# Kernel tuning notes

Measured on AMD Instinct MI355X. Metric: run time of the kernel, lower is better.

The kernel has to match this reference:

```python
import jax, jax.numpy as jnp
import numpy as np

D_MODEL, D_STATE, D_CONV, EXPAND = 1024, 16, 4, 2
D_INNER = EXPAND * D_MODEL
B, L = 2, 4096
LN_EPS = 1e-5


def setup_inputs() -> dict:
    key = jax.random.key(0)
    ks = jax.random.split(key, 6)
    x = jax.random.normal(ks[0], (B, L, D_MODEL), dtype=jnp.float32)
    ln_gamma = jnp.ones((D_MODEL,), jnp.float32)
    ln_beta = jnp.zeros((D_MODEL,), jnp.float32)
    W_in = jax.random.normal(ks[1], (2 * D_INNER, D_MODEL), jnp.float32) / np.sqrt(D_MODEL).astype(np.float32)
    conv_w = jax.random.normal(ks[2], (D_INNER, 1, D_CONV), jnp.float32) * 0.1
    conv_b = jnp.zeros((D_INNER,), jnp.float32)
    W_out = jax.random.normal(ks[3], (D_MODEL, D_INNER), jnp.float32) / np.sqrt(D_INNER).astype(np.float32)
    A = jnp.eye(D_STATE, dtype=jnp.float32)
    Bm = jax.random.normal(ks[4], (D_STATE, D_INNER), jnp.float32) * 0.01
    Cm = jax.random.normal(ks[5], (D_STATE, D_INNER), jnp.float32) * 0.01
    return dict(x=x, ln_gamma=ln_gamma, ln_beta=ln_beta, W_in=W_in,
                conv_w=conv_w, conv_b=conv_b, W_out=W_out, A=A, Bm=Bm, Cm=Cm)


def _layernorm(x, gamma, beta):
    mu = jnp.mean(x, axis=-1, keepdims=True)
    var = jnp.mean(jnp.square(x - mu), axis=-1, keepdims=True)
    return (x - mu) * jax.lax.rsqrt(var + LN_EPS) * gamma + beta


def _causal_depthwise_conv(xp, conv_w, conv_b):
    # xp: (B, L, D_INNER) -> torch Conv1d(padding=K-1, groups=C) then slice [:L]
    # == left-pad K-1, valid depthwise conv.
    lhs = jnp.pad(xp.transpose(0, 2, 1), ((0, 0), (0, 0), (D_CONV - 1, 0)))  # (B,C,L+K-1)
    out = jax.lax.conv_general_dilated(
        lhs, conv_w, window_strides=(1,), padding='VALID',
        dimension_numbers=('NCH', 'OIH', 'NCH'), feature_group_count=D_INNER)
    return out.transpose(0, 2, 1) + conv_b  # (B, L, C)


def reference(x, ln_gamma, ln_beta, W_in, conv_w, conv_b, W_out, A, Bm, Cm):
    # scan permutation is identity (untrained optimizer state); masking disabled
    xn = _layernorm(x, ln_gamma, ln_beta)
    xz = jnp.einsum('bld,ed->ble', xn, W_in)          # (B, L, 2*D_INNER)
    x_part, z = jnp.split(xz, 2, axis=-1)             # each (B, L, D_INNER)
    x_conv = jax.nn.silu(_causal_depthwise_conv(x_part, conv_w, conv_b))

    # recurrence: s_t = s_{t-1} @ A.T + u_t @ B.T ; out_t = (x_conv_t + s_t @ C) * sigmoid(z_t)
    u_seq = x_part.transpose(1, 0, 2)                 # (L, B, D_INNER)
    xc_seq = x_conv.transpose(1, 0, 2)
    z_seq = z.transpose(1, 0, 2)

    def step(state, inp):
        u_t, xc_t, z_t = inp
        state = state @ A.T + u_t @ Bm.T              # (B, D_STATE)
        out = (xc_t + state @ Cm) * jax.nn.sigmoid(z_t)
        return state, out

    state0 = jnp.zeros((x.shape[0], D_STATE), x.dtype)
    _, ys = jax.lax.scan(step, state0, (u_seq, xc_seq, z_seq))
    y = ys.transpose(1, 0, 2)                         # (B, L, D_INNER)
    residual = jnp.einsum('bli,di->bld', y, W_out)    # (B, L, D_MODEL)
    return x + residual
```

## Files before the change

### kernel.cpp

```cpp
#include <hip/hip_runtime.h>
#include <hip/hip_bf16.h>
#include <math.h>

#define D_MODEL 1024
#define D_STATE 16
#define D_CONV 4
#define D_INNER 2048
#define BATCH 2
#define SEQ 4096
#define NROW (BATCH * SEQ)
#define LN_EPS 1e-5f

typedef __attribute__((ext_vector_type(8))) short  bf16x8_t;
typedef __attribute__((ext_vector_type(4))) float  f32x4_t;
typedef __attribute__((ext_vector_type(8))) unsigned short u16x8_t;

__device__ inline unsigned short f2bf(float f) {
    unsigned u = __float_as_uint(f);
    u += 0x7fffu + ((u >> 16) & 1u);
    return (unsigned short)(u >> 16);
}
__device__ inline float bf2f(unsigned short u) {
    return __uint_as_float((unsigned)u << 16);
}

#define GLL16(g, l)                                                            \
    __builtin_amdgcn_global_load_lds(                                          \
        (const __attribute__((address_space(1))) void*)(g),                    \
        (__attribute__((address_space(3))) void*)(l), 16, 0, 0)

#define FENCE asm volatile("" ::: "memory")
#define BAR do { FENCE; __builtin_amdgcn_s_barrier(); FENCE; } while (0)

#define CVT_BLOCKS 3088
__global__ __launch_bounds__(256) void pre_kernel(const float* __restrict__ x,
                                                  const float* __restrict__ gamma,
                                                  const float* __restrict__ beta,
                                                  const float* __restrict__ W_in,
                                                  const float* __restrict__ W_out,
                                                  const float* __restrict__ Bm,
                                                  unsigned short* __restrict__ xn,
                                                  unsigned short* __restrict__ Win_bf,
                                                  unsigned short* __restrict__ Wout_bf,
                                                  unsigned short* __restrict__ Bm_bf) {
    __shared__ float red[8];
    const int tid = threadIdx.x;
    if (blockIdx.x < CVT_BLOCKS) {
        const long long g = (long long)(blockIdx.x * 256 + tid) * 8;
        const long long n1 = (long long)2 * D_INNER * D_MODEL;
        const long long n2 = n1 + (long long)D_MODEL * D_INNER;
        const float* src; unsigned short* dst; long long off;
        if (g < n1)      { src = W_in;  dst = Win_bf;  off = g; }
        else if (g < n2) { src = W_out; dst = Wout_bf; off = g - n1; }
        else             { src = Bm;    dst = Bm_bf;   off = g - n2; }
        const float4 a = *reinterpret_cast<const float4*>(src + off);
        const float4 b = *reinterpret_cast<const float4*>(src + off + 4);
        u16x8_t p;
        p[0] = f2bf(a.x); p[1] = f2bf(a.y); p[2] = f2bf(a.z); p[3] = f2bf(a.w);
        p[4] = f2bf(b.x); p[5] = f2bf(b.y); p[6] = f2bf(b.z); p[7] = f2bf(b.w);
        *reinterpret_cast<u16x8_t*>(dst + off) = p;
        return;
    }
    const int row = blockIdx.x - CVT_BLOCKS;
    const float4* xr = reinterpret_cast<const float4*>(x + (size_t)row * D_MODEL);
    float4 v = xr[tid];

    const int lane = tid & 63, wave = tid >> 6;
    float s = v.x + v.y + v.z + v.w;
    #pragma unroll
    for (int off = 32; off > 0; off >>= 1) s += __shfl_down(s, off, 64);
    if (lane == 0) red[wave] = s;
    __syncthreads();
    float mu = (red[0] + red[1] + red[2] + red[3]) * (1.0f / D_MODEL);
    __syncthreads();

    float dx = v.x - mu, dy = v.y - mu, dz = v.z - mu, dw = v.w - mu;
    float ss = dx * dx + dy * dy + dz * dz + dw * dw;
    #pragma unroll
    for (int off = 32; off > 0; off >>= 1) ss += __shfl_down(ss, off, 64);
    if (lane == 0) red[wave] = ss;
    __syncthreads();
    float var = (red[0] + red[1] + red[2] + red[3]) * (1.0f / D_MODEL);
    float rs = rsqrtf(var + LN_EPS);

    const float4 gv = reinterpret_cast<const float4*>(gamma)[tid];
    const float4 bv = reinterpret_cast<const float4*>(beta)[tid];
    ushort4 o;
    o.x = f2bf(dx * rs * gv.x + bv.x);
    o.y = f2bf(dy * rs * gv.y + bv.y);
    o.z = f2bf(dz * rs * gv.z + bv.z);
    o.w = f2bf(dw * rs * gv.w + bv.w);
    reinterpret_cast<ushort4*>(xn + (size_t)row * D_MODEL)[tid] = o;
}

__global__ __launch_bounds__(512, 2) void gemm256_bf16(const short* __restrict__ A,
                                                       const short* __restrict__ B,
                                                       unsigned short* __restrict__ Cb,
                                                       int M, int N, int K) {
    __shared__ short lds[2 * 4 * 8192];

    const int tid = threadIdx.x;
    const int w = tid >> 6, l = tid & 63;

    const int id = blockIdx.y * gridDim.x + blockIdx.x;
    const int cpx = (gridDim.x * gridDim.y) >> 3;
    const int sid = (id & 7) * cpx + (id >> 3);
    const int row0 = (sid / gridDim.x) * 256;
    const int col0 = (sid % gridDim.x) * 256;

    const int wm = w >> 2;
    const int wn = w & 3;
    const int fr = l & 15;
    const int fc = (l >> 4) * 8;
    const int NT = K >> 6;

    const int qa = wm;
    const int qb = 2 + (wn >> 1);
    const int bb = (wn & 1) * 64;

    auto STAGE = [&](const short* __restrict__ G, int growbase, int k0,
                     int buf, int q) {
        #pragma unroll
        for (int j = 0; j < 2; ++j) {
            const int e = ((j * 8 + w) << 9) + l * 8;
            const int r = e >> 6;
            const int c = (e & 63) ^ ((r & 7) << 3);
            GLL16(G + (size_t)(growbase + r) * K + k0 + c,
                  &lds[buf * 32768 + q * 8192 + ((j * 8 + w) << 9)]);
        }
    };
    auto LDF = [&](int buf, int q, int r, int ks) -> bf16x8_t {
        const int c = (ks * 32 + fc) ^ ((r & 7) << 3);
        return *reinterpret_cast<const bf16x8_t*>(
            &lds[buf * 32768 + q * 8192 + r * 64 + c]);
    };

    f32x4_t acc[8][4] = {};
    bf16x8_t af[4][2], af2[4][2], bA[2][2], bB[2][2];

#define MFMA_Q(AF, mh, nh, BFR)                                                \
    do {                                                                       \
        _Pragma("unroll")                                                      \
        for (int mi = 0; mi < 4; ++mi)                                         \
            _Pragma("unroll")                                                  \
            for (int ni = 0; ni < 2; ++ni)                                     \
                _Pragma("unroll")                                              \
                for (int ks = 0; ks < 2; ++ks)                                 \
                    acc[(mh) * 4 + mi][(nh) * 2 + ni] =                        \
                        __builtin_amdgcn_mfma_f32_16x16x32_bf16(               \
                            AF[mi][ks], BFR[ni][ks],                           \
                            acc[(mh) * 4 + mi][(nh) * 2 + ni], 0, 0, 0);       \
    } while (0)

    STAGE(A, row0,       0, 0, 0);
    STAGE(A, row0 + 128, 0, 0, 1);
    STAGE(B, col0,       0, 0, 2);
    STAGE(B, col0 + 128, 0, 0, 3);
    if (NT > 1) {
        STAGE(B, col0,       64, 1, 2);
        STAGE(B, col0 + 128, 64, 1, 3);
        STAGE(A, row0,       64, 1, 0);
        asm volatile("s_waitcnt vmcnt(6)" ::: "memory");
    } else {
        asm volatile("s_waitcnt vmcnt(0)" ::: "memory");
    }
    BAR;

    for (int kt = 0; kt < NT; ++kt) {
        const int buf = kt & 1, nbuf = buf ^ 1;
        #pragma unroll
        for (int mi = 0; mi < 4; ++mi)
            #pragma unroll
            for (int ks = 0; ks < 2; ++ks)
                af[mi][ks] = LDF(buf, qa, mi * 16 + fr, ks);
        #pragma unroll
        for (int ni = 0; ni < 2; ++ni)
            #pragma unroll
            for (int ks = 0; ks < 2; ++ks)
                bA[ni][ks] = LDF(buf, qb, bb + ni * 16 + fr, ks);
        #pragma unroll
        for (int ni = 0; ni < 2; ++ni)
            #pragma unroll
            for (int ks = 0; ks < 2; ++ks)
                bB[ni][ks] = LDF(buf, qb, bb + 32 + ni * 16 + fr, ks);
        #pragma unroll
        for (int mi = 0; mi < 4; ++mi)
            #pragma unroll
            for (int ks = 0; ks < 2; ++ks)
                af2[mi][ks] = LDF(buf, qa, 64 + mi * 16 + fr, ks);
        if (kt + 1 < NT) STAGE(A, row0 + 128, (kt + 1) << 6, nbuf, 1);
        asm volatile("s_waitcnt lgkmcnt(0)" ::: "memory");
        BAR;
        if (kt + 2 < NT) {
            STAGE(B, col0,       (kt + 2) << 6, buf, 2);
            STAGE(B, col0 + 128, (kt + 2) << 6, buf, 3);
            STAGE(A, row0,       (kt + 2) << 6, buf, 0);
            asm volatile("s_waitcnt vmcnt(6)" ::: "memory");
        } else {
            asm volatile("s_waitcnt vmcnt(0)" ::: "memory");
        }
        BAR;
        __builtin_amdgcn_s_setprio(1);
        MFMA_Q(af,  0, 0, bA);
        MFMA_Q(af,  0, 1, bB);
        MFMA_Q(af2, 1, 1, bB);
        MFMA_Q(af2, 1, 0, bA);
        __builtin_amdgcn_s_setprio(0);
    }
#undef MFMA_Q

    const int cr = (l >> 4) * 4;
    const int cc = l & 15;
    #pragma unroll
    for (int m = 0; m < 8; ++m) {
        #pragma unroll
        for (int n = 0; n < 4; ++n) {
            size_t base = (size_t)(row0 + wm * 128 + m * 16 + cr) * N +
                          (col0 + wn * 64 + n * 16 + cc);
            #pragma unroll
            for (int j = 0; j < 4; ++j)
                Cb[base + (size_t)j * N] = f2bf(acc[m][n][j]);
        }
    }
}

__global__ __launch_bounds__(512) void gemm_out(const short* __restrict__ A,
                                                const short* __restrict__ B,
                                                const float* __restrict__ add,
                                                float* __restrict__ C,
                                                int M, int N, int K) {
    __shared__ short lds[3 * 3 * 8192];

    const int tid = threadIdx.x;
    const int w = tid >> 6, l = tid & 63;

    const int id = blockIdx.y * gridDim.x + blockIdx.x;
    const int cpx = (gridDim.x * gridDim.y) >> 3;
    const int sid = (id & 7) * cpx + (id >> 3);
    const int row0 = (sid / gridDim.x) * 256;
    const int col0 = (sid % gridDim.x) * 128;

    const int wm = w >> 1;
    const int wn = w & 1;
    const int qa = wm >> 1;
    const int lr0 = (wm & 1) * 64;
    const int fr = l & 15;
    const int fc = (l >> 4) * 8;
    const int NT = K >> 6;

    auto STAGE = [&](const short* __restrict__ G, int growbase, int k0,
                     int buf, int q) {
        #pragma unroll
        for (int j = 0; j < 2; ++j) {
            const int e = ((j * 8 + w) << 9) + l * 8;
            const int r = e >> 6;
            const int c = (e & 63) ^ ((r & 7) << 3);
            GLL16(G + (size_t)(growbase + r) * K + k0 + c,
                  &lds[buf * 24576 + q * 8192 + ((j * 8 + w) << 9)]);
        }
    };
    auto LDF = [&](int buf, int q, int r, int ks) -> bf16x8_t {
        const int c = (ks * 32 + fc) ^ ((r & 7) << 3);
        return *reinterpret_cast<const bf16x8_t*>(
            &lds[buf * 24576 + q * 8192 + r * 64 + c]);
    };

    f32x4_t acc[4][4] = {};
    bf16x8_t af[4][2], bf[4][2];

    STAGE(A, row0,       0, 0, 0);
    STAGE(A, row0 + 128, 0, 0, 1);
    STAGE(B, col0,       0, 0, 2);
    if (NT > 1) {
        STAGE(A, row0,       64, 1, 0);
        STAGE(A, row0 + 128, 64, 1, 1);
        STAGE(B, col0,       64, 1, 2);
        asm volatile("s_waitcnt vmcnt(6)" ::: "memory");
    } else {
        asm volatile("s_waitcnt vmcnt(0)" ::: "memory");
    }

    int buf = 0;
    for (int kt = 0; kt < NT; ++kt) {
        BAR;
        #pragma unroll
        for (int mi = 0; mi < 4; ++mi)
            #pragma unroll
            for (int ks = 0; ks < 2; ++ks)
                af[mi][ks] = LDF(buf, qa, lr0 + mi * 16 + fr, ks);
        #pragma unroll
        for (int ni = 0; ni < 4; ++ni)
            #pragma unroll
            for (int ks = 0; ks < 2; ++ks)
                bf[ni][ks] = LDF(buf, 2, wn * 64 + ni * 16 + fr, ks);
        __builtin_amdgcn_s_setprio(1);
        #pragma unroll
        for (int mi = 0; mi < 4; ++mi)
            #pragma unroll
            for (int ni = 0; ni < 4; ++ni)
                #pragma unroll
                for (int ks = 0; ks < 2; ++ks)
                    acc[mi][ni] = __builtin_amdgcn_mfma_f32_16x16x32_bf16(
                        af[mi][ks], bf[ni][ks], acc[mi][ni], 0, 0, 0);
        __builtin_amdgcn_s_setprio(0);
        if (kt + 2 < NT) {
            const int sb = (buf + 2) % 3;
            STAGE(A, row0,       (kt + 2) << 6, sb, 0);
            STAGE(A, row0 + 128, (kt + 2) << 6, sb, 1);
            STAGE(B, col0,       (kt + 2) << 6, sb, 2);
            asm volatile("s_waitcnt vmcnt(6)" ::: "memory");
        } else {
            asm volatile("s_waitcnt vmcnt(0)" ::: "memory");
        }
        buf = (buf + 1) % 3;
    }

    const int cr = (l >> 4) * 4;
    const int cc = l & 15;
    #pragma unroll
    for (int mi = 0; mi < 4; ++mi) {
        #pragma unroll
        for (int ni = 0; ni < 4; ++ni) {
            size_t base = (size_t)(row0 + wm * 64 + mi * 16 + cr) * N +
                          (col0 + wn * 64 + ni * 16 + cc);
            #pragma unroll
            for (int j = 0; j < 4; ++j)
                C[base + (size_t)j * N] = acc[mi][ni][j] + add[base + (size_t)j * N];
        }
    }
}

__global__ __launch_bounds__(64) void v_mfma(const unsigned short* __restrict__ xz,
                                             const unsigned short* __restrict__ Bmb,
                                             float* __restrict__ V) {
    const int l = threadIdx.x;
    const int r0 = blockIdx.x * 16;
    const int fr = l & 15;
    const int fk = (l >> 4) * 8;

    const unsigned short* aP = xz + (size_t)(r0 + fr) * (2 * D_INNER) + fk;
    const unsigned short* bP = Bmb + fr * D_INNER + fk;

    f32x4_t a0 = {}, a1 = {}, a2 = {}, a3 = {};
    #pragma unroll 2
    for (int k0 = 0; k0 < D_INNER; k0 += 128) {
        a0 = __builtin_amdgcn_mfma_f32_16x16x32_bf16(
            *reinterpret_cast<const bf16x8_t*>(aP + k0),
            *reinterpret_cast<const bf16x8_t*>(bP + k0), a0, 0, 0, 0);
        a1 = __builtin_amdgcn_mfma_f32_16x16x32_bf16(
            *reinterpret_cast<const bf16x8_t*>(aP + k0 + 32),
            *reinterpret_cast<const bf16x8_t*>(bP + k0 + 32), a1, 0, 0, 0);
        a2 = __builtin_amdgcn_mfma_f32_16x16x32_bf16(
            *reinterpret_cast<const bf16x8_t*>(aP + k0 + 64),
            *reinterpret_cast<const bf16x8_t*>(bP + k0 + 64), a2, 0, 0, 0);
        a3 = __builtin_amdgcn_mfma_f32_16x16x32_bf16(
            *reinterpret_cast<const bf16x8_t*>(aP + k0 + 96),
            *reinterpret_cast<const bf16x8_t*>(bP + k0 + 96), a3, 0, 0, 0);
    }

    const int cr = (l >> 4) * 4;
    const int cc = l & 15;
    #pragma unroll
    for (int j = 0; j < 4; ++j)
        V[(size_t)(r0 + cr + j) * D_STATE + cc] = a0[j] + a1[j] + a2[j] + a3[j];
}

__global__ __launch_bounds__(256) void scan_par(const float* __restrict__ V,
                                                const float* __restrict__ A,
                                                float* __restrict__ S) {
    __shared__ int nid;
    const int tid = threadIdx.x;
    if (tid == 0) nid = 0;
    __syncthreads();
    {
        const float ex = ((tid >> 4) == (tid & 15)) ? 1.0f : 0.0f;
        if (A[tid] != ex) atomicOr(&nid, 1);
    }
    __syncthreads();
    if (nid) return;

    const int p = blockIdx.x;
    const int b = p >> 4, s = p & 15;
    const float* vb = V + (size_t)b * SEQ * D_STATE + s;
    float* sb = S + (size_t)b * SEQ * D_STATE + s;

    const int t0 = tid * 16;
    float v[16];
    float run = 0.0f;
    #pragma unroll
    for (int j = 0; j < 16; ++j) {
        run += vb[(size_t)(t0 + j) * D_STATE];
        v[j] = run;
    }

    const float tot = run;
    float sc = tot;
    #pragma unroll
    for (int off = 1; off < 64; off <<= 1) {
        float n = __shfl_up(sc, off, 64);
        if ((tid & 63) >= off) sc += n;
    }
    __shared__ float wtot[4];
    if ((tid & 63) == 63) wtot[tid >> 6] = sc;
    __syncthreads();
    float woff = 0.0f;
    #pragma unroll
    for (int w2 = 0; w2 < 4; ++w2)
        if (w2 < (tid >> 6)) woff += wtot[w2];
    const float excl = sc - tot + woff;

    #pragma unroll
    for (int j = 0; j < 16; ++j)
        sb[(size_t)(t0 + j) * D_STATE] = v[j] + excl;
}

#define SCAN_CHUNK 256

__global__ __launch_bounds__(64) void scan_seq(const float* __restrict__ V,
                                               const float* __restrict__ A,
                                               float* __restrict__ S) {
    const int tid = threadIdx.x;
    int bad = 0;
    for (int i = tid; i < D_STATE * D_STATE; i += 64) {
        const float ex = ((i >> 4) == (i & 15)) ? 1.0f : 0.0f;
        if (A[i] != ex) bad = 1;
    }
    if (__ballot(bad) == 0ULL) return;

    __shared__ float Al[D_STATE * D_STATE];
    __shared__ float Vl[2 * SCAN_CHUNK * D_STATE];
    __shared__ float Sl[2 * SCAN_CHUNK * D_STATE];

    for (int i = tid; i < D_STATE * D_STATE; i += 64) Al[i] = A[i];
    __syncthreads();

    float st = 0.0f;
    const int bb = (tid >> 4) & 1;
    const int ss = tid & 15;

    for (int t0 = 0; t0 < SEQ; t0 += SCAN_CHUNK) {
        for (int idx = tid; idx < 2 * SCAN_CHUNK * D_STATE; idx += 64) {
            int b = idx >> 12;
            int rem = idx & 4095;
            Vl[idx] = V[((size_t)(b * SEQ + t0) * D_STATE) + rem];
        }
        __syncthreads();

        if (tid < 32) {
            float* vb = Vl + bb * SCAN_CHUNK * D_STATE + ss;
            float* sb = Sl + bb * SCAN_CHUNK * D_STATE + ss;
            for (int t = 0; t < SCAN_CHUNK; ++t) {
                float ns = vb[t * D_STATE];
                #pragma unroll
                for (int s2 = 0; s2 < D_STATE; ++s2) {
                    float other = __shfl(st, (tid & 16) | s2, 64);
                    ns = fmaf(Al[ss * D_STATE + s2], other, ns);
                }
                st = ns;
                sb[t * D_STATE] = st;
            }
        }
        __syncthreads();

        for (int idx = tid; idx < 2 * SCAN_CHUNK * D_STATE; idx += 64) {
            int b = idx >> 12;
            int rem = idx & 4095;
            S[((size_t)(b * SEQ + t0) * D_STATE) + rem] = Sl[idx];
        }
        __syncthreads();
    }
}

__global__ __launch_bounds__(256) void y_kernel(const unsigned short* __restrict__ xz,
                                                const float* __restrict__ S,
                                                const float* __restrict__ Cm,
                                                const float* __restrict__ convw,
                                                const float* __restrict__ convb,
                                                unsigned short* __restrict__ y) {
    const int tid = threadIdx.x;
    const int i0 = blockIdx.x * 512 + tid * 2;
    const int r0 = blockIdx.y * 64;
    const int tb0 = r0 & (SEQ - 1);

    const float4 w0 = *reinterpret_cast<const float4*>(&convw[i0 * D_CONV]);
    const float4 w1 = *reinterpret_cast<const float4*>(&convw[(i0 + 1) * D_CONV]);
    const float cb0 = convb[i0], cb1 = convb[i0 + 1];
    float cm0[D_STATE], cm1[D_STATE];
    #pragma unroll
    for (int s = 0; s < D_STATE; ++s) {
        float2 c = *reinterpret_cast<const float2*>(&Cm[s * D_INNER + i0]);
        cm0[s] = c.x; cm1[s] = c.y;
    }

    float2 xm1 = make_float2(0.f, 0.f), xm2 = xm1, xm3 = xm1;
    if (tb0 >= 1) { ushort2 u = *reinterpret_cast<const ushort2*>(&xz[(size_t)(r0 - 1) * (2 * D_INNER) + i0]); xm1 = make_float2(bf2f(u.x), bf2f(u.y)); }
    if (tb0 >= 2) { ushort2 u = *reinterpret_cast<const ushort2*>(&xz[(size_t)(r0 - 2) * (2 * D_INNER) + i0]); xm2 = make_float2(bf2f(u.x), bf2f(u.y)); }
    if (tb0 >= 3) { ushort2 u = *reinterpret_cast<const ushort2*>(&xz[(size_t)(r0 - 3) * (2 * D_INNER) + i0]); xm3 = make_float2(bf2f(u.x), bf2f(u.y)); }

    for (int r = r0; r < r0 + 64; ++r) {
        const ushort2 xu = *reinterpret_cast<const ushort2*>(&xz[(size_t)r * (2 * D_INNER) + i0]);
        const ushort2 zu = *reinterpret_cast<const ushort2*>(&xz[(size_t)r * (2 * D_INNER) + D_INNER + i0]);
        const float2 x0 = make_float2(bf2f(xu.x), bf2f(xu.y));

        float a0 = cb0;
        a0 = fmaf(w0.x, xm3.x, a0); a0 = fmaf(w0.y, xm2.x, a0);
        a0 = fmaf(w0.z, xm1.x, a0); a0 = fmaf(w0.w, x0.x, a0);
        float a1 = cb1;
        a1 = fmaf(w1.x, xm3.y, a1); a1 = fmaf(w1.y, xm2.y, a1);
        a1 = fmaf(w1.z, xm1.y, a1); a1 = fmaf(w1.w, x0.y, a1);

        const float xc0 = a0 / (1.0f + expf(-a0));
        const float xc1 = a1 / (1.0f + expf(-a1));

        const float4* Sp = reinterpret_cast<const float4*>(S + (size_t)r * D_STATE);
        const float4 s0 = Sp[0], s1 = Sp[1], s2 = Sp[2], s3 = Sp[3];
        const float sv[D_STATE] = {s0.x, s0.y, s0.z, s0.w, s1.x, s1.y, s1.z, s1.w,
                                   s2.x, s2.y, s2.z, s2.w, s3.x, s3.y, s3.z, s3.w};
        float sc0 = 0.f, sc1 = 0.f;
        #pragma unroll
        for (int s = 0; s < D_STATE; ++s) {
            sc0 = fmaf(sv[s], cm0[s], sc0);
            sc1 = fmaf(sv[s], cm1[s], sc1);
        }

        const float z0 = bf2f(zu.x), z1 = bf2f(zu.y);
        const float g0 = 1.0f / (1.0f + expf(-z0));
        const float g1 = 1.0f / (1.0f + expf(-z1));

        ushort2 o;
        o.x = f2bf((xc0 + sc0) * g0);
        o.y = f2bf((xc1 + sc1) * g1);
        *reinterpret_cast<ushort2*>(&y[(size_t)r * D_INNER + i0]) = o;

        xm3 = xm2; xm2 = xm1; xm1 = x0;
    }
}

extern "C" void kernel_launch(void* const* d_in, const int* in_sizes, int n_in,
                              void* d_out, int out_size, void* d_ws, size_t ws_size,
                              hipStream_t stream) {
    const float* x      = (const float*)d_in[0];
    const float* ln_g   = (const float*)d_in[1];
    const float* ln_b   = (const float*)d_in[2];
    const float* W_in   = (const float*)d_in[3];
    const float* conv_w = (const float*)d_in[4];
    const float* conv_b = (const float*)d_in[5];
    const float* W_out  = (const float*)d_in[6];
    const float* A      = (const float*)d_in[7];
    const float* Bm     = (const float*)d_in[8];
    const float* Cm     = (const float*)d_in[9];
    float* out = (float*)d_out;

    float* ws = (float*)d_ws;
    float* V  = ws;
    float* S  = V + (size_t)NROW * D_STATE;
    unsigned short* xz_bf  = (unsigned short*)(S + (size_t)NROW * D_STATE);
    unsigned short* xn_bf  = xz_bf  + (size_t)NROW * 2 * D_INNER;
    unsigned short* Win_bf = xn_bf  + (size_t)NROW * D_MODEL;
    unsigned short* Wout_bf= Win_bf + (size_t)(2 * D_INNER) * D_MODEL;
    unsigned short* Bm_bf  = Wout_bf + (size_t)D_MODEL * D_INNER;
    unsigned short* y_bf   = Bm_bf  + (size_t)D_STATE * D_INNER;

    pre_kernel<<<CVT_BLOCKS + NROW, 256, 0, stream>>>(
        x, ln_g, ln_b, W_in, W_out, Bm, xn_bf, Win_bf, Wout_bf, Bm_bf);

    gemm256_bf16<<<dim3((2 * D_INNER) / 256, NROW / 256), 512, 0, stream>>>(
        (const short*)xn_bf, (const short*)Win_bf, xz_bf,
        NROW, 2 * D_INNER, D_MODEL);

    v_mfma<<<NROW / 16, 64, 0, stream>>>(xz_bf, Bm_bf, V);

    scan_par<<<32, 256, 0, stream>>>(V, A, S);
    scan_seq<<<1, 64, 0, stream>>>(V, A, S);

    y_kernel<<<dim3(D_INNER / 512, NROW / 64), 256, 0, stream>>>(
        xz_bf, S, Cm, conv_w, conv_b, y_bf);

    gemm_out<<<dim3(D_MODEL / 128, NROW / 256), 512, 0, stream>>>(
        (const short*)y_bf, (const short*)Wout_bf, x, out,
        NROW, D_MODEL, D_INNER);
}
```

Measured before the change: 190.5 us.

## Split v_mfma K across waves, fuse scan kernels, widen y_kernel per thread

v_mfma now runs two waves per block, each covering half the K range, and combines the partial sums through shared memory. This is meant to give more parallelism and shorten each block's serial MFMA chain. The parallel prefix scan and the general sequential-scan fallback are merged into one launch, with block 32 handling the non-identity-A path, which removes a kernel launch. y_kernel now handles four channels per thread with vector loads and stores. That halves the grid and raises register pressure per thread.

After: 211.2 us. +10.8%, slower.

```diff
diff --git a/kernel.cpp b/kernel.cpp
--- a/kernel.cpp
+++ b/kernel.cpp
@@ -330,20 +330,24 @@
     }
 }
 
-__global__ __launch_bounds__(64) void v_mfma(const unsigned short* __restrict__ xz,
-                                             const unsigned short* __restrict__ Bmb,
-                                             float* __restrict__ V) {
-    const int l = threadIdx.x;
+__global__ __launch_bounds__(128) void v_mfma(const unsigned short* __restrict__ xz,
+                                              const unsigned short* __restrict__ Bmb,
+                                              float* __restrict__ V) {
+    __shared__ float part[2][16][16];
+    const int tid = threadIdx.x;
+    const int wv = tid >> 6;
+    const int l = tid & 63;
     const int r0 = blockIdx.x * 16;
     const int fr = l & 15;
     const int fk = (l >> 4) * 8;
-
-    const unsigned short* aP = xz + (size_t)(r0 + fr) * (2 * D_INNER) + fk;
-    const unsigned short* bP = Bmb + fr * D_INNER + fk;
+    const int kbase = wv * (D_INNER / 2);
+
+    const unsigned short* aP = xz + (size_t)(r0 + fr) * (2 * D_INNER) + kbase + fk;
+    const unsigned short* bP = Bmb + fr * D_INNER + kbase + fk;
 
     f32x4_t a0 = {}, a1 = {}, a2 = {}, a3 = {};
     #pragma unroll 2
-    for (int k0 = 0; k0 < D_INNER; k0 += 128) {
+    for (int k0 = 0; k0 < D_INNER / 2; k0 += 128) {
         a0 = __builtin_amdgcn_mfma_f32_16x16x32_bf16(
             *reinterpret_cast<const bf16x8_t*>(aP + k0),
             *reinterpret_cast<const bf16x8_t*>(bP + k0), a0, 0, 0, 0);
@@ -362,14 +366,68 @@
     const int cc = l & 15;
     #pragma unroll
     for (int j = 0; j < 4; ++j)
-        V[(size_t)(r0 + cr + j) * D_STATE + cc] = a0[j] + a1[j] + a2[j] + a3[j];
-}
-
-__global__ __launch_bounds__(256) void scan_par(const float* __restrict__ V,
-                                                const float* __restrict__ A,
-                                                float* __restrict__ S) {
+        part[wv][cr + j][cc] = a0[j] + a1[j] + a2[j] + a3[j];
+    __syncthreads();
+    if (tid < 64) {
+        #pragma unroll
+        for (int j = 0; j < 4; ++j)
+            V[(size_t)(r0 + cr + j) * D_STATE + cc] =
+                part[0][cr + j][cc] + part[1][cr + j][cc];
+    }
+}
+
+#define SCAN_CHUNK 256
+__global__ __launch_bounds__(256) void scan_fused(const float* __restrict__ V,
+                                                  const float* __restrict__ A,
+                                                  float* __restrict__ S) {
+    const int tid = threadIdx.x;
     __shared__ int nid;
-    const int tid = threadIdx.x;
+    if (blockIdx.x < 32) {
+        if (tid == 0) nid = 0;
+        __syncthreads();
+        {
+            const float ex = ((tid >> 4) == (tid & 15)) ? 1.0f : 0.0f;
+            if (A[tid] != ex) atomicOr(&nid, 1);
+        }
+        __syncthreads();
+        if (nid) return;
+
+        const int p = blockIdx.x;
+        const int b = p >> 4, s = p & 15;
+        const float* vb = V + (size_t)b * SEQ * D_STATE + s;
+        float* sb = S + (size_t)b * SEQ * D_STATE + s;
+
+        const int t0 = tid * 16;
+        float v[16];
+        float run = 0.0f;
+        #pragma unroll
+        for (int j = 0; j < 16; ++j) {
+            run += vb[(size_t)(t0 + j) * D_STATE];
+            v[j] = run;
+        }
+
+        const float tot = run;
+        float sc = tot;
+        #pragma unroll
+        for (int off = 1; off < 64; off <<= 1) {
+            float n = __shfl_up(sc, off, 64);
+            if ((tid & 63) >= off) sc += n;
+        }
+        __shared__ float wtot[4];
+        if ((tid & 63) == 63) wtot[tid >> 6] = sc;
+        __syncthreads();
+        float woff = 0.0f;
+        #pragma unroll
+        for (int w2 = 0; w2 < 4; ++w2)
+            if (w2 < (tid >> 6)) woff += wtot[w2];
+        const float excl = sc - tot + woff;
+
+        #pragma unroll
+        for (int j = 0; j < 16; ++j)
+            sb[(size_t)(t0 + j) * D_STATE] = v[j] + excl;
+        return;
+    }
+
     if (tid == 0) nid = 0;
     __syncthreads();
     {
@@ -377,61 +435,13 @@
         if (A[tid] != ex) atomicOr(&nid, 1);
     }
     __syncthreads();
-    if (nid) return;
-
-    const int p = blockIdx.x;
-    const int b = p >> 4, s = p & 15;
-    const float* vb = V + (size_t)b * SEQ * D_STATE + s;
-    float* sb = S + (size_t)b * SEQ * D_STATE + s;
-
-    const int t0 = tid * 16;
-    float v[16];
-    float run = 0.0f;
-    #pragma unroll
-    for (int j = 0; j < 16; ++j) {
-        run += vb[(size_t)(t0 + j) * D_STATE];
-        v[j] = run;
-    }
-
-    const float tot = run;
-    float sc = tot;
-    #pragma unroll
-    for (int off = 1; off < 64; off <<= 1) {
-        float n = __shfl_up(sc, off, 64);
-        if ((tid & 63) >= off) sc += n;
-    }
-    __shared__ float wtot[4];
-    if ((tid & 63) == 63) wtot[tid >> 6] = sc;
-    __syncthreads();
-    float woff = 0.0f;
-    #pragma unroll
-    for (int w2 = 0; w2 < 4; ++w2)
-        if (w2 < (tid >> 6)) woff += wtot[w2];
-    const float excl = sc - tot + woff;
-
-    #pragma unroll
-    for (int j = 0; j < 16; ++j)
-        sb[(size_t)(t0 + j) * D_STATE] = v[j] + excl;
-}
-
-#define SCAN_CHUNK 256
-
-__global__ __launch_bounds__(64) void scan_seq(const float* __restrict__ V,
-                                               const float* __restrict__ A,
-                                               float* __restrict__ S) {
-    const int tid = threadIdx.x;
-    int bad = 0;
-    for (int i = tid; i < D_STATE * D_STATE; i += 64) {
-        const float ex = ((i >> 4) == (i & 15)) ? 1.0f : 0.0f;
-        if (A[i] != ex) bad = 1;
-    }
-    if (__ballot(bad) == 0ULL) return;
+    if (nid == 0) return;
 
     __shared__ float Al[D_STATE * D_STATE];
     __shared__ float Vl[2 * SCAN_CHUNK * D_STATE];
     __shared__ float Sl[2 * SCAN_CHUNK * D_STATE];
 
-    for (int i = tid; i < D_STATE * D_STATE; i += 64) Al[i] = A[i];
+    Al[tid] = A[tid];
     __syncthreads();
 
     float st = 0.0f;
@@ -439,7 +449,7 @@
     const int ss = tid & 15;
 
     for (int t0 = 0; t0 < SEQ; t0 += SCAN_CHUNK) {
-        for (int idx = tid; idx < 2 * SCAN_CHUNK * D_STATE; idx += 64) {
+        for (int idx = tid; idx < 2 * SCAN_CHUNK * D_STATE; idx += 256) {
             int b = idx >> 12;
             int rem = idx & 4095;
             Vl[idx] = V[((size_t)(b * SEQ + t0) * D_STATE) + rem];
@@ -462,7 +472,7 @@
         }
         __syncthreads();
 
-        for (int idx = tid; idx < 2 * SCAN_CHUNK * D_STATE; idx += 64) {
+        for (int idx = tid; idx < 2 * SCAN_CHUNK * D_STATE; idx += 256) {
             int b = idx >> 12;
             int rem = idx & 4095;
             S[((size_t)(b * SEQ + t0) * D_STATE) + rem] = Sl[idx];
@@ -478,61 +488,58 @@
                                                 const float* __restrict__ convb,
                                                 unsigned short* __restrict__ y) {
     const int tid = threadIdx.x;
-    const int i0 = blockIdx.x * 512 + tid * 2;
+    const int i0 = blockIdx.x * 1024 + tid * 4;
     const int r0 = blockIdx.y * 64;
     const int tb0 = r0 & (SEQ - 1);
 
-    const float4 w0 = *reinterpret_cast<const float4*>(&convw[i0 * D_CONV]);
-    const float4 w1 = *reinterpret_cast<const float4*>(&convw[(i0 + 1) * D_CONV]);
-    const float cb0 = convb[i0], cb1 = convb[i0 + 1];
-    float cm0[D_STATE], cm1[D_STATE];
+    float4 w[4];
+    #pragma unroll
+    for (int c = 0; c < 4; ++c)
+        w[c] = *reinterpret_cast<const float4*>(&convw[(i0 + c) * D_CONV]);
+    const float4 cb = *reinterpret_cast<const float4*>(&convb[i0]);
+    const float cbv[4] = {cb.x, cb.y, cb.z, cb.w};
+    float cm[4][D_STATE];
     #pragma unroll
     for (int s = 0; s < D_STATE; ++s) {
-        float2 c = *reinterpret_cast<const float2*>(&Cm[s * D_INNER + i0]);
-        cm0[s] = c.x; cm1[s] = c.y;
-    }
-
-    float2 xm1 = make_float2(0.f, 0.f), xm2 = xm1, xm3 = xm1;
-    if (tb0 >= 1) { ushort2 u = *reinterpret_cast<const ushort2*>(&xz[(size_t)(r0 - 1) * (2 * D_INNER) + i0]); xm1 = make_float2(bf2f(u.x), bf2f(u.y)); }
-    if (tb0 >= 2) { ushort2 u = *reinterpret_cast<const ushort2*>(&xz[(size_t)(r0 - 2) * (2 * D_INNER) + i0]); xm2 = make_float2(bf2f(u.x), bf2f(u.y)); }
-    if (tb0 >= 3) { ushort2 u = *reinterpret_cast<const ushort2*>(&xz[(size_t)(r0 - 3) * (2 * D_INNER) + i0]); xm3 = make_float2(bf2f(u.x), bf2f(u.y)); }
+        float4 c = *reinterpret_cast<const float4*>(&Cm[s * D_INNER + i0]);
+        cm[0][s] = c.x; cm[1][s] = c.y; cm[2][s] = c.z; cm[3][s] = c.w;
+    }
+
+    float xm1[4] = {}, xm2[4] = {}, xm3[4] = {};
+    if (tb0 >= 1) { ushort4 u = *reinterpret_cast<const ushort4*>(&xz[(size_t)(r0 - 1) * (2 * D_INNER) + i0]);
+                    xm1[0] = bf2f(u.x); xm1[1] = bf2f(u.y); xm1[2] = bf2f(u.z); xm1[3] = bf2f(u.w); }
+    if (tb0 >= 2) { ushort4 u = *reinterpret_cast<const ushort4*>(&xz[(size_t)(r0 - 2) * (2 * D_INNER) + i0]);
+                    xm2[0] = bf2f(u.x); xm2[1] = bf2f(u.y); xm2[2] = bf2f(u.z); xm2[3] = bf2f(u.w); }
+    if (tb0 >= 3) { ushort4 u = *reinterpret_cast<const ushort4*>(&xz[(size_t)(r0 - 3) * (2 * D_INNER) + i0]);
+                    xm3[0] = bf2f(u.x); xm3[1] = bf2f(u.y); xm3[2] = bf2f(u.z); xm3[3] = bf2f(u.w); }
 
     for (int r = r0; r < r0 + 64; ++r) {
-        const ushort2 xu = *reinterpret_cast<const ushort2*>(&xz[(size_t)r * (2 * D_INNER) + i0]);
-        const ushort2 zu = *reinterpret_cast<const ushort2*>(&xz[(size_t)r * (2 * D_INNER) + D_INNER + i0]);
-        const float2 x0 = make_float2(bf2f(xu.x), bf2f(xu.y));
-
-        float a0 = cb0;
-        a0 = fmaf(w0.x, xm3.x, a0); a0 = fmaf(w0.y, xm2.x, a0);
-        a0 = fmaf(w0.z, xm1.x, a0); a0 = fmaf(w0.w, x0.x, a0);
-        float a1 = cb1;
-        a1 = fmaf(w1.x, xm3.y, a1); a1 = fmaf(w1.y, xm2.y, a1);
-        a1 = fmaf(w1.z, xm1.y, a1); a1 = fmaf(w1.w, x0.y, a1);
-
-        const float xc0 = a0 / (1.0f + expf(-a0));
-        const float xc1 = a1 / (1.0f + expf(-a1));
+        const ushort4 xu = *reinterpret_cast<const ushort4*>(&xz[(size_t)r * (2 * D_INNER) + i0]);
+        const ushort4 zu = *reinterpret_cast<const ushort4*>(&xz[(size_t)r * (2 * D_INNER) + D_INNER + i0]);
+        const float x0[4] = {bf2f(xu.x), bf2f(xu.y), bf2f(xu.z), bf2f(xu.w)};
+        const float zv[4] = {bf2f(zu.x), bf2f(zu.y), bf2f(zu.z), bf2f(zu.w)};
 
         const float4* Sp = reinterpret_cast<const float4*>(S + (size_t)r * D_STATE);
         const float4 s0 = Sp[0], s1 = Sp[1], s2 = Sp[2], s3 = Sp[3];
         const float sv[D_STATE] = {s0.x, s0.y, s0.z, s0.w, s1.x, s1.y, s1.z, s1.w,
                                    s2.x, s2.y, s2.z, s2.w, s3.x, s3.y, s3.z, s3.w};
-        float sc0 = 0.f, sc1 = 0.f;
-        #pragma unroll
-        for (int s = 0; s < D_STATE; ++s) {
-            sc0 = fmaf(sv[s], cm0[s], sc0);
-            sc1 = fmaf(sv[s], cm1[s], sc1);
-        }
-
-        const float z0 = bf2f(zu.x), z1 = bf2f(zu.y);
-        const float g0 = 1.0f / (1.0f + expf(-z0));
-        const float g1 = 1.0f / (1.0f + expf(-z1));
-
-        ushort2 o;
-        o.x = f2bf((xc0 + sc0) * g0);
-        o.y = f2bf((xc1 + sc1) * g1);
-        *reinterpret_cast<ushort2*>(&y[(size_t)r * D_INNER + i0]) = o;
-
-        xm3 = xm2; xm2 = xm1; xm1 = x0;
+
+        ushort4 o;
+        unsigned short* op = reinterpret_cast<unsigned short*>(&o);
+        #pragma unroll
+        for (int c = 0; c < 4; ++c) {
+            float a = cbv[c];
+            a = fmaf(w[c].x, xm3[c], a); a = fmaf(w[c].y, xm2[c], a);
+            a = fmaf(w[c].z, xm1[c], a); a = fmaf(w[c].w, x0[c], a);
+            const float xc = a / (1.0f + expf(-a));
+            float sc = 0.f;
+            #pragma unroll
+            for (int s = 0; s < D_STATE; ++s) sc = fmaf(sv[s], cm[c][s], sc);
+            const float g = 1.0f / (1.0f + expf(-zv[c]));
+            op[c] = f2bf((xc + sc) * g);
+            xm3[c] = xm2[c]; xm2[c] = xm1[c]; xm1[c] = x0[c];
+        }
+        *reinterpret_cast<ushort4*>(&y[(size_t)r * D_INNER + i0]) = o;
     }
 }
 
@@ -568,12 +575,11 @@
         (const short*)xn_bf, (const short*)Win_bf, xz_bf,
         NROW, 2 * D_INNER, D_MODEL);
 
-    v_mfma<<<NROW / 16, 64, 0, stream>>>(xz_bf, Bm_bf, V);
-
-    scan_par<<<32, 256, 0, stream>>>(V, A, S);
-    scan_seq<<<1, 64, 0, stream>>>(V, A, S);
-
-    y_kernel<<<dim3(D_INNER / 512, NROW / 64), 256, 0, stream>>>(
+    v_mfma<<<NROW / 16, 128, 0, stream>>>(xz_bf, Bm_bf, V);
+
+    scan_fused<<<33, 256, 0, stream>>>(V, A, S);
+
+    y_kernel<<<dim3(D_INNER / 1024, NROW / 64), 256, 0, stream>>>(
         xz_bf, S, Cm, conv_w, conv_b, y_bf);
 
     gemm_out<<<dim3(D_MODEL / 128, NROW / 256), 512, 0, stream>>>(
```
